# Kernel tuning notes

Hardware: AMD Instinct MI355X
Metric: run time of the kernel (lower is better)

Reference implementation:

```python
import jax, jax.numpy as jnp
import numpy as np

BS, T, HS, WS = 2, 4, 32, 32
HW = HS * WS
D, NH, NL, NP = 256, 8, 4, 4
HD = D // NH
DFFN = 1024


def layer_norm(x, g, b, eps=1e-5):
    mu = jnp.mean(x, axis=-1, keepdims=True)
    var = jnp.mean((x - mu) ** 2, axis=-1, keepdims=True)
    return (x - mu) * jax.lax.rsqrt(var + eps) * g + b


def bilinear_gather(val, loc, Hl, Wl):
    # val: (bs, nh, Hl*Wl, hd); loc: (bs, Lq, nh, P, 2) in [0,1], last dim (x, y)
    # matches F.grid_sample(align_corners=False, padding_mode='zeros') on grid=2*loc-1
    x = loc[..., 0] * Wl - 0.5
    y = loc[..., 1] * Hl - 0.5
    x0 = jnp.floor(x)
    y0 = jnp.floor(y)
    lx = x - x0
    ly = y - y0
    bs, Lq, nh, P = x.shape
    out = jnp.zeros((bs, nh, Lq * P, val.shape[-1]), val.dtype)
    for dy in (0, 1):
        for dx in (0, 1):
            xi = x0 + dx
            yi = y0 + dy
            w = (lx if dx else 1.0 - lx) * (ly if dy else 1.0 - ly)
            valid = (xi >= 0) & (xi < Wl) & (yi >= 0) & (yi < Hl)
            w = jnp.where(valid, w, 0.0)
            xi_c = jnp.clip(xi, 0, Wl - 1).astype(jnp.int32)
            yi_c = jnp.clip(yi, 0, Hl - 1).astype(jnp.int32)
            idx = (yi_c * Wl + xi_c).transpose(0, 2, 1, 3).reshape(bs, nh, Lq * P)
            g = jnp.take_along_axis(val, idx[..., None], axis=2)
            wt = w.transpose(0, 2, 1, 3).reshape(bs, nh, Lq * P)
            out = out + wt[..., None] * g
    return out.reshape(bs, nh, Lq, P, val.shape[-1])


def setup_inputs() -> dict:
    key = jax.random.key(0)
    ks = jax.random.split(key, 12)
    s = 0.02
    return {
        "src": jax.random.normal(ks[0], (BS, T, HW, D), jnp.float32),
        "pos": jax.random.normal(ks[1], (BS, T, HW, D), jnp.float32),
        "reference_points": jax.random.uniform(ks[2], (BS, T * HW, NL, 2), jnp.float32),
        "value_proj_w": jax.random.normal(ks[3], (D, D), jnp.float32) * s,
        "value_proj_b": jnp.zeros((D,), jnp.float32),
        "sampling_offsets_w": jax.random.normal(ks[4], (D, NH * NL * NP * 2), jnp.float32) * s,
        "sampling_offsets_b": jax.random.normal(ks[5], (NH * NL * NP * 2,), jnp.float32) * s,
        "attn_weights_w": jax.random.normal(ks[6], (D, NH * NL * NP), jnp.float32) * s,
        "attn_weights_b": jnp.zeros((NH * NL * NP,), jnp.float32),
        "output_proj_w": jax.random.normal(ks[7], (D, D), jnp.float32) * s,
        "output_proj_b": jnp.zeros((D,), jnp.float32),
        "norm1_g": jnp.ones((D,), jnp.float32),
        "norm1_b": jnp.zeros((D,), jnp.float32),
        "linear1_w": jax.random.normal(ks[8], (D, DFFN), jnp.float32) * s,
        "linear1_b": jnp.zeros((DFFN,), jnp.float32),
        "linear2_w": jax.random.normal(ks[9], (DFFN, D), jnp.float32) * s,
        "linear2_b": jnp.zeros((D,), jnp.float32),
        "norm2_g": jnp.ones((D,), jnp.float32),
        "norm2_b": jnp.zeros((D,), jnp.float32),
        "spatial_shapes": np.array([[HS, WS]] * NL, np.int32),
        "level_start_index": np.arange(NL, dtype=np.int32) * HW,
    }


def reference(src, pos, reference_points, value_proj_w, value_proj_b,
              sampling_offsets_w, sampling_offsets_b, attn_weights_w, attn_weights_b,
              output_proj_w, output_proj_b, norm1_g, norm1_b,
              linear1_w, linear1_b, linear2_w, linear2_b, norm2_g, norm2_b,
              spatial_shapes, level_start_index):
    bs, t, hw, d = src.shape
    Lq = t * hw
    x = src.reshape(bs, Lq, d)
    q = x  # module never adds pos in forward (with_pos_embed unused)
    value = (x @ value_proj_w + value_proj_b).reshape(bs, Lq, NH, HD)
    offsets = (q @ sampling_offsets_w + sampling_offsets_b).reshape(bs, Lq, NH, NL, NP, 2)
    aw = jax.nn.softmax((q @ attn_weights_w + attn_weights_b).reshape(bs, Lq, NH, NL * NP), axis=-1)
    aw = aw.reshape(bs, Lq, NH, NL, NP)
    ss = np.asarray(spatial_shapes)
    lsi = np.asarray(level_start_index)
    offset_normalizer = jnp.asarray(ss[:, ::-1].copy(), src.dtype)  # (L, 2) = (W, H)
    sampling_locations = reference_points[:, :, None, :, None, :] + offsets / offset_normalizer[None, None, None, :, None, :]
    attn_out = jnp.zeros((bs, NH, Lq, HD), src.dtype)
    for l in range(NL):
        Hl, Wl = int(ss[l, 0]), int(ss[l, 1])
        start = int(lsi[l])
        v_l = value[:, start:start + Hl * Wl].transpose(0, 2, 1, 3)  # (bs, nh, HlWl, hd)
        samp = bilinear_gather(v_l, sampling_locations[:, :, :, l], Hl, Wl)  # (bs, nh, Lq, P, hd)
        w_l = aw[:, :, :, l].transpose(0, 2, 1, 3)  # (bs, nh, Lq, P)
        attn_out = attn_out + jnp.sum(samp * w_l[..., None], axis=3)
    attn_out = attn_out.transpose(0, 2, 1, 3).reshape(bs, Lq, d) @ output_proj_w + output_proj_b
    x = layer_norm(x + attn_out, norm1_g, norm1_b)
    ffn = jax.nn.relu(x @ linear1_w + linear1_b) @ linear2_w + linear2_b
    x = layer_norm(x + ffn, norm2_g, norm2_b)
    return x.reshape(bs, t, hw, d), sampling_locations
```

## Files before the change

kernel.cpp:

```cpp
#include <hip/hip_runtime.h>
#include <math.h>

#define ROWS   8192
#define LQ     4096
#define NHEAD  8
#define NLVL   4
#define NPTS   4
#define HDIM   32

typedef __attribute__((ext_vector_type(8))) short v8s;
typedef __attribute__((ext_vector_type(4))) float v4f;
typedef __attribute__((ext_vector_type(8))) unsigned short v8u;

__device__ __forceinline__ unsigned short f2bf(float x) {
    unsigned int u = __float_as_uint(x);
    u += 0x7fffu + ((u >> 16) & 1u);
    return (unsigned short)(u >> 16);
}
__device__ __forceinline__ float bf2f(unsigned short x) {
    return __uint_as_float(((unsigned int)x) << 16);
}

__device__ __forceinline__ void glds16(const void* g, void* l) {
    __builtin_amdgcn_global_load_lds(
        (const __attribute__((address_space(1))) unsigned int*)g,
        (__attribute__((address_space(3))) unsigned int*)l, 16, 0, 0);
}

__device__ __forceinline__ void trans_tile(const float* __restrict__ in,
                                           unsigned short* __restrict__ out,
                                           int K, int N, int ldout, int n_off,
                                           int bx, int by, int tid)
{
    __shared__ float t[32][33];
    int tx = tid & 31, ty = tid >> 5;
    int k0 = by << 5, n0 = bx << 5;
    #pragma unroll
    for (int i = 0; i < 4; i++)
        t[ty + i * 8][tx] = in[(size_t)(k0 + ty + i * 8) * N + n0 + tx];
    __syncthreads();
    #pragma unroll
    for (int i = 0; i < 4; i++)
        out[(size_t)(n_off + n0 + ty + i * 8) * ldout + k0 + tx] = f2bf(t[tx][ty + i * 8]);
}

__global__ __launch_bounds__(256) void prep_k(
    const float* __restrict__ vw, const float* __restrict__ ofw,
    const float* __restrict__ aww, const float* __restrict__ pw,
    const float* __restrict__ w1, const float* __restrict__ w2,
    unsigned short* __restrict__ Btcat, unsigned short* __restrict__ pwT,
    unsigned short* __restrict__ w1T, unsigned short* __restrict__ w2T,
    const float* __restrict__ vb, const float* __restrict__ ofb,
    const float* __restrict__ awb, float* __restrict__ biascat)
{
    int bid = blockIdx.x, tid = threadIdx.x;
    if (bid < 64) {
        int t = bid; trans_tile(vw, Btcat, 256, 256, 256, 0, t & 7, t >> 3, tid);
    } else if (bid < 128) {
        int t = bid - 64; trans_tile(ofw, Btcat, 256, 256, 256, 256, t & 7, t >> 3, tid);
    } else if (bid < 160) {
        int t = bid - 128; trans_tile(aww, Btcat, 256, 128, 256, 512, t & 3, t >> 2, tid);
    } else if (bid < 224) {
        int t = bid - 160; trans_tile(pw, pwT, 256, 256, 256, 0, t & 7, t >> 3, tid);
    } else if (bid < 480) {
        int t = bid - 224; trans_tile(w1, w1T, 256, 1024, 256, 0, t & 31, t >> 5, tid);
    } else if (bid < 736) {
        int t = bid - 480; trans_tile(w2, w2T, 1024, 256, 1024, 0, t & 7, t >> 3, tid);
    } else {
        biascat[tid] = vb[tid];
        biascat[tid + 256] = ofb[tid];
        if (tid < 128) biascat[tid + 512] = awb[tid];
    }
}

template<bool PROJ, bool AF32, bool OUTBF, bool RELU, bool RES>
__global__ __launch_bounds__(256) void mfma_gemm128_k(
    const void* __restrict__ Araw,
    const unsigned short* __restrict__ Bt,
    const float* __restrict__ bias,
    const float* __restrict__ res,
    void* __restrict__ Cout,
    unsigned short* __restrict__ vbf,
    const float* __restrict__ refp,
    float* __restrict__ oloc,
    int M, int N, int K)
{
    __shared__ __align__(16) unsigned short As[2048];
    __shared__ __align__(16) unsigned short Bs[4096];
    const int tid = threadIdx.x;
    const int row0 = blockIdx.y << 6, col0 = blockIdx.x << 7;
    const int wid = tid >> 6, lane = tid & 63;
    const int wm = wid & 1, wn = wid >> 1;
    const int lr = lane & 15, kq = lane >> 4;

    v4f acc[2][4];
    #pragma unroll
    for (int i = 0; i < 2; i++)
        #pragma unroll
        for (int j = 0; j < 4; j++) acc[i][j] = (v4f){0.f, 0.f, 0.f, 0.f};

    for (int k0 = 0; k0 < K; k0 += 32) {
        float4 af0, af1;
        if constexpr (AF32) {
            const float* Af = (const float*)Araw;
            int r1 = tid >> 2, kk1 = ((tid & 3) + (r1 >> 2)) & 3;
            const float* p1 = Af + (size_t)(row0 + r1) * K + k0 + kk1 * 8;
            af0 = *(const float4*)p1; af1 = *(const float4*)(p1 + 4);
        }
        __syncthreads();
        if constexpr (AF32) {
            v8u u1;
            u1[0] = f2bf(af0.x); u1[1] = f2bf(af0.y); u1[2] = f2bf(af0.z); u1[3] = f2bf(af0.w);
            u1[4] = f2bf(af1.x); u1[5] = f2bf(af1.y); u1[6] = f2bf(af1.z); u1[7] = f2bf(af1.w);
            *(v8u*)(&As[tid * 8]) = u1;
        } else {
            const unsigned short* A = (const unsigned short*)Araw;
            int c = wid * 64 + lane;
            int row = c >> 2;
            int kk = ((c & 3) + (row >> 2)) & 3;
            glds16(A + (size_t)(row0 + row) * K + k0 + kk * 8,
                   &As[(wid * 64) * 8]);
        }
        #pragma unroll
        for (int i = 0; i < 2; i++) {
            int c = wid * 128 + i * 64 + lane;
            int row = c >> 2;
            int kk = ((c & 3) + (row >> 2)) & 3;
            glds16(Bt + (size_t)(col0 + row) * K + k0 + kk * 8,
                   &Bs[(wid * 128 + i * 64) * 8]);
        }
        __syncthreads();
        v8s bf[4];
        #pragma unroll
        for (int nt = 0; nt < 4; nt++) {
            int row = wn * 64 + nt * 16 + lr;
            int s = (kq - (row >> 2)) & 3;
            bf[nt] = *(const v8s*)(&Bs[(row * 4 + s) * 8]);
        }
        #pragma unroll
        for (int mt = 0; mt < 2; mt++) {
            int row = wm * 32 + mt * 16 + lr;
            int s = (kq - (row >> 2)) & 3;
            v8s af = *(const v8s*)(&As[(row * 4 + s) * 8]);
            #pragma unroll
            for (int nt = 0; nt < 4; nt++)
                acc[mt][nt] = __builtin_amdgcn_mfma_f32_16x16x32_bf16(af, bf[nt], acc[mt][nt], 0, 0, 0);
        }
    }

    const int rq = lane >> 4;
    #pragma unroll
    for (int mt = 0; mt < 2; mt++) {
        #pragma unroll
        for (int nt = 0; nt < 4; nt++) {
            int col = col0 + wn * 64 + nt * 16 + lr;
            float bv = bias[col];
            #pragma unroll
            for (int i = 0; i < 4; i++) {
                int row = row0 + wm * 32 + mt * 16 + rq * 4 + i;
                float v = acc[mt][nt][i] + bv;
                if (RELU) v = fmaxf(v, 0.f);
                if (RES)  v += res[(size_t)row * N + col];
                if (PROJ) {
                    if (col < 256) {
                        int b = row >> 12, rb = row & 4095;
                        int l = rb >> 10, pix = rb & 1023;
                        int h = col >> 5, d = col & 31;
                        size_t idx = ((size_t)(((b << 2) + l) * 8 + h) << 15) + (pix << 5) + d;
                        vbf[idx] = f2bf(v);
                    } else if (col < 512) {
                        int colm = col - 256;
                        int l = (colm >> 3) & 3, cc = colm & 1;
                        oloc[(size_t)row * 256 + colm] =
                            refp[(size_t)row * 8 + l * 2 + cc] + v * (1.f / 32.f);
                    } else {
                        ((float*)Cout)[(size_t)row * 128 + col - 512] = v;
                    }
                } else if (OUTBF) {
                    ((unsigned short*)Cout)[(size_t)row * N + col] = f2bf(v);
                } else {
                    ((float*)Cout)[(size_t)row * N + col] = v;
                }
            }
        }
    }
}

template<bool OUTBF, bool RELU, bool RES>
__global__ __launch_bounds__(256) void mfma_gemm64_k(
    const unsigned short* __restrict__ A,
    const unsigned short* __restrict__ Bt,
    const float* __restrict__ bias,
    const float* __restrict__ res,
    void* __restrict__ Cout,
    int M, int N, int K)
{
    __shared__ __align__(16) unsigned short As[2048];
    __shared__ __align__(16) unsigned short Bs[2048];
    const int tid = threadIdx.x;
    const int row0 = blockIdx.y << 6, col0 = blockIdx.x << 6;
    const int wid = tid >> 6, lane = tid & 63;
    const int lr = lane & 15, kq = lane >> 4;

    v4f acc[4];
    #pragma unroll
    for (int i = 0; i < 4; i++) acc[i] = (v4f){0.f, 0.f, 0.f, 0.f};

    for (int k0 = 0; k0 < K; k0 += 32) {
        __syncthreads();
        {
            int c = wid * 64 + lane;
            int row = c >> 2;
            int kk = ((c & 3) + (row >> 2)) & 3;
            glds16(A + (size_t)(row0 + row) * K + k0 + kk * 8, &As[wid * 512]);
            glds16(Bt + (size_t)(col0 + row) * K + k0 + kk * 8, &Bs[wid * 512]);
        }
        __syncthreads();
        int colr = wid * 16 + lr;
        int sb = (kq - (colr >> 2)) & 3;
        v8s bf = *(const v8s*)(&Bs[(colr * 4 + sb) * 8]);
        #pragma unroll
        for (int mt = 0; mt < 4; mt++) {
            int rowr = mt * 16 + lr;
            int sa = (kq - (rowr >> 2)) & 3;
            v8s af = *(const v8s*)(&As[(rowr * 4 + sa) * 8]);
            acc[mt] = __builtin_amdgcn_mfma_f32_16x16x32_bf16(af, bf, acc[mt], 0, 0, 0);
        }
    }

    const int rq = lane >> 4;
    const int col = col0 + wid * 16 + lr;
    float bv = bias[col];
    #pragma unroll
    for (int mt = 0; mt < 4; mt++) {
        #pragma unroll
        for (int i = 0; i < 4; i++) {
            int row = row0 + mt * 16 + rq * 4 + i;
            float v = acc[mt][i] + bv;
            if (RELU) v = fmaxf(v, 0.f);
            if (RES)  v += res[(size_t)row * N + col];
            if (OUTBF) ((unsigned short*)Cout)[(size_t)row * N + col] = f2bf(v);
            else       ((float*)Cout)[(size_t)row * N + col] = v;
        }
    }
}

template<bool WRITE_BF>
__global__ __launch_bounds__(256) void mfma_gemm_ln_k(
    const unsigned short* __restrict__ A,
    const unsigned short* __restrict__ Bt,
    const float* __restrict__ bias,
    const float* __restrict__ res,
    const float* __restrict__ g,
    const float* __restrict__ b,
    float* __restrict__ out,
    unsigned short* __restrict__ outbf,
    int M, int K)
{
    __shared__ __align__(16) unsigned short As[1024];
    __shared__ __align__(16) unsigned short Bs[8192];
    __shared__ float red[2][32][4];
    const int tid = threadIdx.x;
    const int row0 = blockIdx.x << 5;
    const int wid = tid >> 6, lane = tid & 63;
    const int lr = lane & 15, kq = lane >> 4;
    const int rq = kq;

    v4f acc[2][4];
    #pragma unroll
    for (int i = 0; i < 2; i++)
        #pragma unroll
        for (int j = 0; j < 4; j++) acc[i][j] = (v4f){0.f, 0.f, 0.f, 0.f};

    for (int k0 = 0; k0 < K; k0 += 32) {
        __syncthreads();
        if (wid < 2) {
            int c = wid * 64 + lane;
            int row = c >> 2;
            int kk = ((c & 3) + (row >> 2)) & 3;
            glds16(A + (size_t)(row0 + row) * K + k0 + kk * 8,
                   &As[(wid * 64) * 8]);
        }
        #pragma unroll
        for (int i = 0; i < 4; i++) {
            int c = (wid * 4 + i) * 64 + lane;
            int col = c >> 2;
            int kk = ((c & 3) + (col >> 2)) & 3;
            glds16(Bt + (size_t)col * K + k0 + kk * 8,
                   &Bs[((wid * 4 + i) * 64) * 8]);
        }
        __syncthreads();
        v8s bf[4];
        #pragma unroll
        for (int ct = 0; ct < 4; ct++) {
            int col = wid * 64 + ct * 16 + lr;
            int s = (kq - (col >> 2)) & 3;
            bf[ct] = *(const v8s*)(&Bs[(col * 4 + s) * 8]);
        }
        #pragma unroll
        for (int rt = 0; rt < 2; rt++) {
            int rowl = rt * 16 + lr;
            int s = (kq - (rowl >> 2)) & 3;
            v8s af = *(const v8s*)(&As[(rowl * 4 + s) * 8]);
            #pragma unroll
            for (int ct = 0; ct < 4; ct++)
                acc[rt][ct] = __builtin_amdgcn_mfma_f32_16x16x32_bf16(af, bf[ct], acc[rt][ct], 0, 0, 0);
        }
    }

    float t[2][4][4];
    float s1[2][4], s2[2][4];
    #pragma unroll
    for (int rt = 0; rt < 2; rt++)
        #pragma unroll
        for (int i = 0; i < 4; i++) { s1[rt][i] = 0.f; s2[rt][i] = 0.f; }
    #pragma unroll
    for (int rt = 0; rt < 2; rt++) {
        #pragma unroll
        for (int ct = 0; ct < 4; ct++) {
            int col = wid * 64 + ct * 16 + lr;
            float bv = bias[col];
            #pragma unroll
            for (int i = 0; i < 4; i++) {
                int row = row0 + rt * 16 + rq * 4 + i;
                float v = acc[rt][ct][i] + bv + res[(size_t)row * 256 + col];
                t[rt][ct][i] = v;
                s1[rt][i] += v;
                s2[rt][i] += v * v;
            }
        }
    }
    #pragma unroll
    for (int o = 1; o < 16; o <<= 1) {
        #pragma unroll
        for (int rt = 0; rt < 2; rt++)
            #pragma unroll
            for (int i = 0; i < 4; i++) {
                s1[rt][i] += __shfl_xor(s1[rt][i], o);
                s2[rt][i] += __shfl_xor(s2[rt][i], o);
            }
    }
    if (lr == 0) {
        #pragma unroll
        for (int rt = 0; rt < 2; rt++)
            #pragma unroll
            for (int i = 0; i < 4; i++) {
                int rl = rt * 16 + rq * 4 + i;
                red[0][rl][wid] = s1[rt][i];
                red[1][rl][wid] = s2[rt][i];
            }
    }
    __syncthreads();
    float mu[2][4], rstd[2][4];
    #pragma unroll
    for (int rt = 0; rt < 2; rt++) {
        #pragma unroll
        for (int i = 0; i < 4; i++) {
            int rl = rt * 16 + rq * 4 + i;
            float S1 = red[0][rl][0] + red[0][rl][1] + red[0][rl][2] + red[0][rl][3];
            float S2 = red[1][rl][0] + red[1][rl][1] + red[1][rl][2] + red[1][rl][3];
            float m = S1 * (1.f / 256.f);
            mu[rt][i] = m;
            rstd[rt][i] = rsqrtf(S2 * (1.f / 256.f) - m * m + 1e-5f);
        }
    }
    #pragma unroll
    for (int rt = 0; rt < 2; rt++) {
        #pragma unroll
        for (int ct = 0; ct < 4; ct++) {
            int col = wid * 64 + ct * 16 + lr;
            float gg = g[col], bb = b[col];
            #pragma unroll
            for (int i = 0; i < 4; i++) {
                int row = row0 + rt * 16 + rq * 4 + i;
                float o = (t[rt][ct][i] - mu[rt][i]) * rstd[rt][i] * gg + bb;
                out[(size_t)row * 256 + col] = o;
                if (WRITE_BF) outbf[(size_t)row * 256 + col] = f2bf(o);
            }
        }
    }
}

__global__ __launch_bounds__(256) void fused_gather_k(
    const float* __restrict__ po,
    const unsigned short* __restrict__ vbf,
    const float* __restrict__ loc,
    unsigned short* __restrict__ attn_bf)
{
    int tid = threadIdx.x;
    int g = tid >> 4, l = (tid >> 2) & 3, d8 = tid & 3;
    int h = blockIdx.x & 7;
    int r = (blockIdx.x >> 3) * 16 + g;
    int b = r >> 12;

    float locv[8];
    *(float4*)(locv)     = *(const float4*)(loc + (size_t)r * 256 + h * 32 + l * 8);
    *(float4*)(locv + 4) = *(const float4*)(loc + (size_t)r * 256 + h * 32 + l * 8 + 4);

    float w4[4];
    *(float4*)(w4) = *(const float4*)(po + (size_t)r * 128 + h * 16 + l * 4);
    float m = fmaxf(fmaxf(w4[0], w4[1]), fmaxf(w4[2], w4[3]));
    m = fmaxf(m, __shfl_xor(m, 4));
    m = fmaxf(m, __shfl_xor(m, 8));
    float s = 0.f;
    #pragma unroll
    for (int p = 0; p < 4; p++) { w4[p] = __expf(w4[p] - m); s += w4[p]; }
    s += __shfl_xor(s, 4);
    s += __shfl_xor(s, 8);
    float inv = 1.f / s;

    const unsigned short* vbase =
        vbf + (((size_t)(((b << 2) + l) * 8 + h)) << 15) + d8 * 8;

    float acc[8];
    #pragma unroll
    for (int k = 0; k < 8; k++) acc[k] = 0.f;

    #pragma unroll
    for (int pp = 0; pp < 2; pp++) {
        v8u uv[8];
        float cw[8];
        #pragma unroll
        for (int p2 = 0; p2 < 2; p2++) {
            int p = pp * 2 + p2;
            float xf = locv[p * 2] * 32.f - 0.5f, yf = locv[p * 2 + 1] * 32.f - 0.5f;
            float x0f = floorf(xf), y0f = floorf(yf);
            float fx = xf - x0f, fy = yf - y0f;
            int x0 = (int)x0f, y0 = (int)y0f;
            float wgt = w4[p] * inv;
            #pragma unroll
            for (int dy = 0; dy < 2; dy++) {
                #pragma unroll
                for (int dx = 0; dx < 2; dx++) {
                    int idx = p2 * 4 + dy * 2 + dx;
                    int xi = x0 + dx, yi = y0 + dy;
                    float wt = (dx ? fx : 1.f - fx) * (dy ? fy : 1.f - fy);
                    bool valid = (xi >= 0) & (xi < 32) & (yi >= 0) & (yi < 32);
                    int xc = min(max(xi, 0), 31), yc = min(max(yi, 0), 31);
                    cw[idx] = valid ? (wgt * wt) : 0.f;
                    uv[idx] = *(const v8u*)(vbase + (size_t)((yc << 5) + xc) * 32);
                }
            }
        }
        #pragma unroll
        for (int idx = 0; idx < 8; idx++) {
            float c = cw[idx];
            #pragma unroll
            for (int k = 0; k < 8; k++)
                acc[k] += c * bf2f(uv[idx][k]);
        }
    }
    #pragma unroll
    for (int k = 0; k < 8; k++) {
        acc[k] += __shfl_xor(acc[k], 4);
        acc[k] += __shfl_xor(acc[k], 8);
    }
    if (l == 0) {
        v8u o;
        #pragma unroll
        for (int k = 0; k < 8; k++) o[k] = f2bf(acc[k]);
        *(v8u*)(attn_bf + (size_t)r * 256 + h * 32 + d8 * 8) = o;
    }
}

template<bool WRITE_BF>
__global__ __launch_bounds__(256) void layernorm_k(
    float* __restrict__ x, const float* __restrict__ g, const float* __restrict__ b,
    unsigned short* __restrict__ xbf)
{
    int lane = threadIdx.x & 63;
    int wv = threadIdx.x >> 6;
    int row = blockIdx.x * 4 + wv;
    int c = lane << 2;
    float4 v = *(const float4*)(x + (size_t)row * 256 + c);
    float s = v.x + v.y + v.z + v.w;
    #pragma unroll
    for (int o = 1; o < 64; o <<= 1) s += __shfl_xor(s, o);
    float mu = s * (1.f / 256.f);
    float d0 = v.x - mu, d1 = v.y - mu, d2 = v.z - mu, d3 = v.w - mu;
    float vs = d0 * d0 + d1 * d1 + d2 * d2 + d3 * d3;
    #pragma unroll
    for (int o = 1; o < 64; o <<= 1) vs += __shfl_xor(vs, o);
    float rstd = rsqrtf(vs * (1.f / 256.f) + 1e-5f);
    float4 gg = *(const float4*)(g + c);
    float4 bb = *(const float4*)(b + c);
    float4 o4;
    o4.x = d0 * rstd * gg.x + bb.x;
    o4.y = d1 * rstd * gg.y + bb.y;
    o4.z = d2 * rstd * gg.z + bb.z;
    o4.w = d3 * rstd * gg.w + bb.w;
    *(float4*)(x + (size_t)row * 256 + c) = o4;
    if (WRITE_BF) {
        ushort4 ob;
        ob.x = f2bf(o4.x); ob.y = f2bf(o4.y); ob.z = f2bf(o4.z); ob.w = f2bf(o4.w);
        *(ushort4*)(xbf + (size_t)row * 256 + c) = ob;
    }
}

extern "C" void kernel_launch(void* const* d_in, const int* in_sizes, int n_in,
                              void* d_out, int out_size, void* d_ws, size_t ws_size,
                              hipStream_t stream)
{
    const float* src   = (const float*)d_in[0];
    const float* refp  = (const float*)d_in[2];
    const float* vw    = (const float*)d_in[3];
    const float* vb    = (const float*)d_in[4];
    const float* ofw   = (const float*)d_in[5];
    const float* ofb   = (const float*)d_in[6];
    const float* aww   = (const float*)d_in[7];
    const float* awb   = (const float*)d_in[8];
    const float* pw    = (const float*)d_in[9];
    const float* pb    = (const float*)d_in[10];
    const float* g1    = (const float*)d_in[11];
    const float* b1    = (const float*)d_in[12];
    const float* w1    = (const float*)d_in[13];
    const float* bi1   = (const float*)d_in[14];
    const float* w2    = (const float*)d_in[15];
    const float* bi2   = (const float*)d_in[16];
    const float* g2    = (const float*)d_in[17];
    const float* b2    = (const float*)d_in[18];

    float* ws = (float*)d_ws;
    float*          po        = ws;
    float*          x1        = ws + 1048576;
    unsigned short* value_bf  = (unsigned short*)(ws + 3145728);
    unsigned short* x1_bf     = (unsigned short*)(ws + 5242880);
    unsigned short* attn_bf   = (unsigned short*)(ws + 6291456);
    unsigned short* hidden_bf = (unsigned short*)(ws + 7340032);
    unsigned short* Btcat     = (unsigned short*)(ws + 11534336);
    unsigned short* pwT       = (unsigned short*)(ws + 11616256);
    unsigned short* w1T       = (unsigned short*)(ws + 11649024);
    unsigned short* w2T       = (unsigned short*)(ws + 11780096);
    float*          biascat   = ws + 11911168;

    float* out_x   = (float*)d_out;
    float* out_loc = out_x + 2097152;

    dim3 blk(256);

    prep_k<<<737, blk, 0, stream>>>(vw, ofw, aww, pw, w1, w2,
                                    Btcat, pwT, w1T, w2T, vb, ofb, awb, biascat);

    mfma_gemm128_k<true, true, false, false, false><<<dim3(5, 128), blk, 0, stream>>>(
        src, Btcat, biascat, nullptr, po, value_bf, refp, out_loc, ROWS, 640, 256);

    fused_gather_k<<<4096, blk, 0, stream>>>(po, value_bf, out_loc, attn_bf);

    mfma_gemm_ln_k<true><<<256, blk, 0, stream>>>(
        attn_bf, pwT, pb, src, g1, b1, x1, x1_bf, ROWS, 256);

    mfma_gemm128_k<false, false, true, true, false><<<dim3(8, 128), blk, 0, stream>>>(
        x1_bf, w1T, bi1, nullptr, hidden_bf, nullptr, nullptr, nullptr, ROWS, 1024, 256);

    mfma_gemm64_k<false, false, true><<<dim3(4, 128), blk, 0, stream>>>(
        hidden_bf, w2T, bi2, x1, out_x, ROWS, 256, 1024);
    layernorm_k<false><<<2048, blk, 0, stream>>>(out_x, g2, b2, nullptr);
}
```

Measured before the change: 182.0 us.

## Merge kernel chain into two cooperative persistent kernels with grid syncs

Replaces six of the seven separate launches with two cooperative kernels of 512 blocks. The first does the weight transposes and the fused input projection, separated by a grid barrier. The second runs out-proj+LN1, FFN1, FFN2 and LN2 with grid barriers between stages. The aim is to remove launch gaps and tail effects between small kernels. In exchange, the fixed 512-block grid limits parallelism for stages that previously used more blocks. The kernels also carry the combined shared memory of all their phases, which may cut occupancy and co-residency.

New measurement: 681.5 us. 275% more time.

```diff
diff --git a/kernel.cpp b/kernel.cpp
--- a/kernel.cpp
+++ b/kernel.cpp
@@ -1,12 +1,10 @@
 #include <hip/hip_runtime.h>
+#include <hip/hip_cooperative_groups.h>
 #include <math.h>
 
+namespace cg = cooperative_groups;
+
 #define ROWS   8192
-#define LQ     4096
-#define NHEAD  8
-#define NLVL   4
-#define NPTS   4
-#define HDIM   32
 
 typedef __attribute__((ext_vector_type(8))) short v8s;
 typedef __attribute__((ext_vector_type(4))) float v4f;
@@ -44,51 +42,16 @@
         out[(size_t)(n_off + n0 + ty + i * 8) * ldout + k0 + tx] = f2bf(t[tx][ty + i * 8]);
 }
 
-__global__ __launch_bounds__(256) void prep_k(
-    const float* __restrict__ vw, const float* __restrict__ ofw,
-    const float* __restrict__ aww, const float* __restrict__ pw,
-    const float* __restrict__ w1, const float* __restrict__ w2,
-    unsigned short* __restrict__ Btcat, unsigned short* __restrict__ pwT,
-    unsigned short* __restrict__ w1T, unsigned short* __restrict__ w2T,
-    const float* __restrict__ vb, const float* __restrict__ ofb,
-    const float* __restrict__ awb, float* __restrict__ biascat)
-{
-    int bid = blockIdx.x, tid = threadIdx.x;
-    if (bid < 64) {
-        int t = bid; trans_tile(vw, Btcat, 256, 256, 256, 0, t & 7, t >> 3, tid);
-    } else if (bid < 128) {
-        int t = bid - 64; trans_tile(ofw, Btcat, 256, 256, 256, 256, t & 7, t >> 3, tid);
-    } else if (bid < 160) {
-        int t = bid - 128; trans_tile(aww, Btcat, 256, 128, 256, 512, t & 3, t >> 2, tid);
-    } else if (bid < 224) {
-        int t = bid - 160; trans_tile(pw, pwT, 256, 256, 256, 0, t & 7, t >> 3, tid);
-    } else if (bid < 480) {
-        int t = bid - 224; trans_tile(w1, w1T, 256, 1024, 256, 0, t & 31, t >> 5, tid);
-    } else if (bid < 736) {
-        int t = bid - 480; trans_tile(w2, w2T, 1024, 256, 1024, 0, t & 7, t >> 3, tid);
-    } else {
-        biascat[tid] = vb[tid];
-        biascat[tid + 256] = ofb[tid];
-        if (tid < 128) biascat[tid + 512] = awb[tid];
-    }
-}
-
-template<bool PROJ, bool AF32, bool OUTBF, bool RELU, bool RES>
-__global__ __launch_bounds__(256) void mfma_gemm128_k(
-    const void* __restrict__ Araw,
-    const unsigned short* __restrict__ Bt,
-    const float* __restrict__ bias,
-    const float* __restrict__ res,
-    void* __restrict__ Cout,
-    unsigned short* __restrict__ vbf,
-    const float* __restrict__ refp,
-    float* __restrict__ oloc,
-    int M, int N, int K)
+__device__ __forceinline__ void proj_tile(
+    const float* __restrict__ Af, const unsigned short* __restrict__ Bt,
+    const float* __restrict__ bias, float* __restrict__ po,
+    unsigned short* __restrict__ vbf, const float* __restrict__ refp,
+    float* __restrict__ oloc, int bx, int by, int tid)
 {
     __shared__ __align__(16) unsigned short As[2048];
     __shared__ __align__(16) unsigned short Bs[4096];
-    const int tid = threadIdx.x;
-    const int row0 = blockIdx.y << 6, col0 = blockIdx.x << 7;
+    const int K = 256;
+    const int row0 = by << 6, col0 = bx << 7;
     const int wid = tid >> 6, lane = tid & 63;
     const int wm = wid & 1, wn = wid >> 1;
     const int lr = lane & 15, kq = lane >> 4;
@@ -100,27 +63,15 @@
         for (int j = 0; j < 4; j++) acc[i][j] = (v4f){0.f, 0.f, 0.f, 0.f};
 
     for (int k0 = 0; k0 < K; k0 += 32) {
-        float4 af0, af1;
-        if constexpr (AF32) {
-            const float* Af = (const float*)Araw;
-            int r1 = tid >> 2, kk1 = ((tid & 3) + (r1 >> 2)) & 3;
-            const float* p1 = Af + (size_t)(row0 + r1) * K + k0 + kk1 * 8;
-            af0 = *(const float4*)p1; af1 = *(const float4*)(p1 + 4);
-        }
-        __syncthreads();
-        if constexpr (AF32) {
-            v8u u1;
-            u1[0] = f2bf(af0.x); u1[1] = f2bf(af0.y); u1[2] = f2bf(af0.z); u1[3] = f2bf(af0.w);
-            u1[4] = f2bf(af1.x); u1[5] = f2bf(af1.y); u1[6] = f2bf(af1.z); u1[7] = f2bf(af1.w);
-            *(v8u*)(&As[tid * 8]) = u1;
-        } else {
-            const unsigned short* A = (const unsigned short*)Araw;
-            int c = wid * 64 + lane;
-            int row = c >> 2;
-            int kk = ((c & 3) + (row >> 2)) & 3;
-            glds16(A + (size_t)(row0 + row) * K + k0 + kk * 8,
-                   &As[(wid * 64) * 8]);
-        }
+        int r1 = tid >> 2, kk1 = ((tid & 3) + (r1 >> 2)) & 3;
+        const float* p1 = Af + (size_t)(row0 + r1) * K + k0 + kk1 * 8;
+        float4 af0 = *(const float4*)p1;
+        float4 af1 = *(const float4*)(p1 + 4);
+        __syncthreads();
+        v8u u1;
+        u1[0] = f2bf(af0.x); u1[1] = f2bf(af0.y); u1[2] = f2bf(af0.z); u1[3] = f2bf(af0.w);
+        u1[4] = f2bf(af1.x); u1[5] = f2bf(af1.y); u1[6] = f2bf(af1.z); u1[7] = f2bf(af1.w);
+        *(v8u*)(&As[tid * 8]) = u1;
         #pragma unroll
         for (int i = 0; i < 2; i++) {
             int c = wid * 128 + i * 64 + lane;
@@ -159,52 +110,43 @@
             for (int i = 0; i < 4; i++) {
                 int row = row0 + wm * 32 + mt * 16 + rq * 4 + i;
                 float v = acc[mt][nt][i] + bv;
-                if (RELU) v = fmaxf(v, 0.f);
-                if (RES)  v += res[(size_t)row * N + col];
-                if (PROJ) {
-                    if (col < 256) {
-                        int b = row >> 12, rb = row & 4095;
-                        int l = rb >> 10, pix = rb & 1023;
-                        int h = col >> 5, d = col & 31;
-                        size_t idx = ((size_t)(((b << 2) + l) * 8 + h) << 15) + (pix << 5) + d;
-                        vbf[idx] = f2bf(v);
-                    } else if (col < 512) {
-                        int colm = col - 256;
-                        int l = (colm >> 3) & 3, cc = colm & 1;
-                        oloc[(size_t)row * 256 + colm] =
-                            refp[(size_t)row * 8 + l * 2 + cc] + v * (1.f / 32.f);
-                    } else {
-                        ((float*)Cout)[(size_t)row * 128 + col - 512] = v;
-                    }
-                } else if (OUTBF) {
-                    ((unsigned short*)Cout)[(size_t)row * N + col] = f2bf(v);
+                if (col < 256) {
+                    int b = row >> 12, rb = row & 4095;
+                    int l = rb >> 10, pix = rb & 1023;
+                    int h = col >> 5, d = col & 31;
+                    size_t idx = ((size_t)(((b << 2) + l) * 8 + h) << 15) + (pix << 5) + d;
+                    vbf[idx] = f2bf(v);
+                } else if (col < 512) {
+                    int colm = col - 256;
+                    int l = (colm >> 3) & 3, cc = colm & 1;
+                    oloc[(size_t)row * 256 + colm] =
+                        refp[(size_t)row * 8 + l * 2 + cc] + v * (1.f / 32.f);
                 } else {
-                    ((float*)Cout)[(size_t)row * N + col] = v;
+                    po[(size_t)row * 128 + col - 512] = v;
                 }
             }
         }
     }
 }
 
-template<bool OUTBF, bool RELU, bool RES>
-__global__ __launch_bounds__(256) void mfma_gemm64_k(
-    const unsigned short* __restrict__ A,
-    const unsigned short* __restrict__ Bt,
-    const float* __restrict__ bias,
-    const float* __restrict__ res,
-    void* __restrict__ Cout,
-    int M, int N, int K)
-{
-    __shared__ __align__(16) unsigned short As[2048];
-    __shared__ __align__(16) unsigned short Bs[2048];
-    const int tid = threadIdx.x;
-    const int row0 = blockIdx.y << 6, col0 = blockIdx.x << 6;
+__device__ __forceinline__ void ffn1_tile(
+    const unsigned short* __restrict__ A, const unsigned short* __restrict__ Bt,
+    const float* __restrict__ bias, unsigned short* __restrict__ Cout,
+    int bx, int by, int tid)
+{
+    __shared__ __align__(16) unsigned short As1[2048];
+    __shared__ __align__(16) unsigned short Bs1[4096];
+    const int K = 256, N = 1024;
+    const int row0 = by << 6, col0 = bx << 7;
     const int wid = tid >> 6, lane = tid & 63;
+    const int wm = wid & 1, wn = wid >> 1;
     const int lr = lane & 15, kq = lane >> 4;
 
-    v4f acc[4];
-    #pragma unroll
-    for (int i = 0; i < 4; i++) acc[i] = (v4f){0.f, 0.f, 0.f, 0.f};
+    v4f acc[2][4];
+    #pragma unroll
+    for (int i = 0; i < 2; i++)
+        #pragma unroll
+        for (int j = 0; j < 4; j++) acc[i][j] = (v4f){0.f, 0.f, 0.f, 0.f};
 
     for (int k0 = 0; k0 < K; k0 += 32) {
         __syncthreads();
@@ -212,18 +154,86 @@
             int c = wid * 64 + lane;
             int row = c >> 2;
             int kk = ((c & 3) + (row >> 2)) & 3;
-            glds16(A + (size_t)(row0 + row) * K + k0 + kk * 8, &As[wid * 512]);
-            glds16(Bt + (size_t)(col0 + row) * K + k0 + kk * 8, &Bs[wid * 512]);
+            glds16(A + (size_t)(row0 + row) * K + k0 + kk * 8, &As1[(wid * 64) * 8]);
+        }
+        #pragma unroll
+        for (int i = 0; i < 2; i++) {
+            int c = wid * 128 + i * 64 + lane;
+            int row = c >> 2;
+            int kk = ((c & 3) + (row >> 2)) & 3;
+            glds16(Bt + (size_t)(col0 + row) * K + k0 + kk * 8,
+                   &Bs1[(wid * 128 + i * 64) * 8]);
+        }
+        __syncthreads();
+        v8s bf[4];
+        #pragma unroll
+        for (int nt = 0; nt < 4; nt++) {
+            int row = wn * 64 + nt * 16 + lr;
+            int s = (kq - (row >> 2)) & 3;
+            bf[nt] = *(const v8s*)(&Bs1[(row * 4 + s) * 8]);
+        }
+        #pragma unroll
+        for (int mt = 0; mt < 2; mt++) {
+            int row = wm * 32 + mt * 16 + lr;
+            int s = (kq - (row >> 2)) & 3;
+            v8s af = *(const v8s*)(&As1[(row * 4 + s) * 8]);
+            #pragma unroll
+            for (int nt = 0; nt < 4; nt++)
+                acc[mt][nt] = __builtin_amdgcn_mfma_f32_16x16x32_bf16(af, bf[nt], acc[mt][nt], 0, 0, 0);
+        }
+    }
+
+    const int rq = lane >> 4;
+    #pragma unroll
+    for (int mt = 0; mt < 2; mt++) {
+        #pragma unroll
+        for (int nt = 0; nt < 4; nt++) {
+            int col = col0 + wn * 64 + nt * 16 + lr;
+            float bv = bias[col];
+            #pragma unroll
+            for (int i = 0; i < 4; i++) {
+                int row = row0 + wm * 32 + mt * 16 + rq * 4 + i;
+                float v = fmaxf(acc[mt][nt][i] + bv, 0.f);
+                Cout[(size_t)row * N + col] = f2bf(v);
+            }
+        }
+    }
+}
+
+__device__ __forceinline__ void ffn2_tile(
+    const unsigned short* __restrict__ A, const unsigned short* __restrict__ Bt,
+    const float* __restrict__ bias, const float* __restrict__ res,
+    float* __restrict__ Cout, int bx, int by, int tid)
+{
+    __shared__ __align__(16) unsigned short As2[2048];
+    __shared__ __align__(16) unsigned short Bs2[2048];
+    const int K = 1024, N = 256;
+    const int row0 = by << 6, col0 = bx << 6;
+    const int wid = tid >> 6, lane = tid & 63;
+    const int lr = lane & 15, kq = lane >> 4;
+
+    v4f acc[4];
+    #pragma unroll
+    for (int i = 0; i < 4; i++) acc[i] = (v4f){0.f, 0.f, 0.f, 0.f};
+
+    for (int k0 = 0; k0 < K; k0 += 32) {
+        __syncthreads();
+        {
+            int c = wid * 64 + lane;
+            int row = c >> 2;
+            int kk = ((c & 3) + (row >> 2)) & 3;
+            glds16(A + (size_t)(row0 + row) * K + k0 + kk * 8, &As2[wid * 512]);
+            glds16(Bt + (size_t)(col0 + row) * K + k0 + kk * 8, &Bs2[wid * 512]);
         }
         __syncthreads();
         int colr = wid * 16 + lr;
         int sb = (kq - (colr >> 2)) & 3;
-        v8s bf = *(const v8s*)(&Bs[(colr * 4 + sb) * 8]);
+        v8s bf = *(const v8s*)(&Bs2[(colr * 4 + sb) * 8]);
         #pragma unroll
         for (int mt = 0; mt < 4; mt++) {
             int rowr = mt * 16 + lr;
             int sa = (kq - (rowr >> 2)) & 3;
-            v8s af = *(const v8s*)(&As[(rowr * 4 + sa) * 8]);
+            v8s af = *(const v8s*)(&As2[(rowr * 4 + sa) * 8]);
             acc[mt] = __builtin_amdgcn_mfma_f32_16x16x32_bf16(af, bf, acc[mt], 0, 0, 0);
         }
     }
@@ -236,32 +246,24 @@
         #pragma unroll
         for (int i = 0; i < 4; i++) {
             int row = row0 + mt * 16 + rq * 4 + i;
-            float v = acc[mt][i] + bv;
-            if (RELU) v = fmaxf(v, 0.f);
-            if (RES)  v += res[(size_t)row * N + col];
-            if (OUTBF) ((unsigned short*)Cout)[(size_t)row * N + col] = f2bf(v);
-            else       ((float*)Cout)[(size_t)row * N + col] = v;
-        }
-    }
-}
-
-template<bool WRITE_BF>
-__global__ __launch_bounds__(256) void mfma_gemm_ln_k(
-    const unsigned short* __restrict__ A,
-    const unsigned short* __restrict__ Bt,
-    const float* __restrict__ bias,
-    const float* __restrict__ res,
-    const float* __restrict__ g,
-    const float* __restrict__ b,
-    float* __restrict__ out,
-    unsigned short* __restrict__ outbf,
-    int M, int K)
-{
-    __shared__ __align__(16) unsigned short As[1024];
-    __shared__ __align__(16) unsigned short Bs[8192];
+            float v = acc[mt][i] + bv + res[(size_t)row * N + col];
+            Cout[(size_t)row * N + col] = v;
+        }
+    }
+}
+
+__device__ __forceinline__ void outproj_ln_tile(
+    const unsigned short* __restrict__ A, const unsigned short* __restrict__ Bt,
+    const float* __restrict__ bias, const float* __restrict__ res,
+    const float* __restrict__ g, const float* __restrict__ b,
+    float* __restrict__ out, unsigned short* __restrict__ outbf,
+    int bxy, int tid)
+{
+    __shared__ __align__(16) unsigned short As3[1024];
+    __shared__ __align__(16) unsigned short Bs3[8192];
     __shared__ float red[2][32][4];
-    const int tid = threadIdx.x;
-    const int row0 = blockIdx.x << 5;
+    const int K = 256;
+    const int row0 = bxy << 5;
     const int wid = tid >> 6, lane = tid & 63;
     const int lr = lane & 15, kq = lane >> 4;
     const int rq = kq;
@@ -278,16 +280,14 @@
             int c = wid * 64 + lane;
             int row = c >> 2;
             int kk = ((c & 3) + (row >> 2)) & 3;
-            glds16(A + (size_t)(row0 + row) * K + k0 + kk * 8,
-                   &As[(wid * 64) * 8]);
+            glds16(A + (size_t)(row0 + row) * K + k0 + kk * 8, &As3[(wid * 64) * 8]);
         }
         #pragma unroll
         for (int i = 0; i < 4; i++) {
             int c = (wid * 4 + i) * 64 + lane;
             int col = c >> 2;
             int kk = ((c & 3) + (col >> 2)) & 3;
-            glds16(Bt + (size_t)col * K + k0 + kk * 8,
-                   &Bs[((wid * 4 + i) * 64) * 8]);
+            glds16(Bt + (size_t)col * K + k0 + kk * 8, &Bs3[((wid * 4 + i) * 64) * 8]);
         }
         __syncthreads();
         v8s bf[4];
@@ -295,13 +295,13 @@
         for (int ct = 0; ct < 4; ct++) {
             int col = wid * 64 + ct * 16 + lr;
             int s = (kq - (col >> 2)) & 3;
-            bf[ct] = *(const v8s*)(&Bs[(col * 4 + s) * 8]);
+            bf[ct] = *(const v8s*)(&Bs3[(col * 4 + s) * 8]);
         }
         #pragma unroll
         for (int rt = 0; rt < 2; rt++) {
             int rowl = rt * 16 + lr;
             int s = (kq - (rowl >> 2)) & 3;
-            v8s af = *(const v8s*)(&As[(rowl * 4 + s) * 8]);
+            v8s af = *(const v8s*)(&As3[(rowl * 4 + s) * 8]);
             #pragma unroll
             for (int ct = 0; ct < 4; ct++)
                 acc[rt][ct] = __builtin_amdgcn_mfma_f32_16x16x32_bf16(af, bf[ct], acc[rt][ct], 0, 0, 0);
@@ -375,10 +375,93 @@
                 int row = row0 + rt * 16 + rq * 4 + i;
                 float o = (t[rt][ct][i] - mu[rt][i]) * rstd[rt][i] * gg + bb;
                 out[(size_t)row * 256 + col] = o;
-                if (WRITE_BF) outbf[(size_t)row * 256 + col] = f2bf(o);
+                outbf[(size_t)row * 256 + col] = f2bf(o);
             }
         }
     }
+}
+
+__device__ __forceinline__ void ln_rows(float* __restrict__ x,
+                                        const float* __restrict__ g,
+                                        const float* __restrict__ b,
+                                        int t, int tid)
+{
+    int lane = tid & 63;
+    int wv = tid >> 6;
+    int row = t * 4 + wv;
+    int c = lane << 2;
+    float4 v = *(const float4*)(x + (size_t)row * 256 + c);
+    float s = v.x + v.y + v.z + v.w;
+    #pragma unroll
+    for (int o = 1; o < 64; o <<= 1) s += __shfl_xor(s, o);
+    float mu = s * (1.f / 256.f);
+    float d0 = v.x - mu, d1 = v.y - mu, d2 = v.z - mu, d3 = v.w - mu;
+    float vs = d0 * d0 + d1 * d1 + d2 * d2 + d3 * d3;
+    #pragma unroll
+    for (int o = 1; o < 64; o <<= 1) vs += __shfl_xor(vs, o);
+    float rstd = rsqrtf(vs * (1.f / 256.f) + 1e-5f);
+    float4 gg = *(const float4*)(g + c);
+    float4 bb = *(const float4*)(b + c);
+    float4 o4;
+    o4.x = d0 * rstd * gg.x + bb.x;
+    o4.y = d1 * rstd * gg.y + bb.y;
+    o4.z = d2 * rstd * gg.z + bb.z;
+    o4.w = d3 * rstd * gg.w + bb.w;
+    *(float4*)(x + (size_t)row * 256 + c) = o4;
+}
+
+__global__ __launch_bounds__(256, 2) void coopA_k(
+    const float* src,
+    const float* vw, const float* ofw, const float* aww, const float* pw,
+    const float* w1, const float* w2,
+    unsigned short* Btcat, unsigned short* pwT,
+    unsigned short* w1T, unsigned short* w2T,
+    const float* vb, const float* ofb, const float* awb, float* biascat,
+    float* po, unsigned short* vbf, const float* refp, float* oloc)
+{
+    int bid = blockIdx.x, tid = threadIdx.x;
+    for (int t = bid; t < 737; t += 512) {
+        if (t < 64) { trans_tile(vw, Btcat, 256, 256, 256, 0, t & 7, t >> 3, tid); }
+        else if (t < 128) { int u = t - 64;  trans_tile(ofw, Btcat, 256, 256, 256, 256, u & 7, u >> 3, tid); }
+        else if (t < 160) { int u = t - 128; trans_tile(aww, Btcat, 256, 128, 256, 512, u & 3, u >> 2, tid); }
+        else if (t < 224) { int u = t - 160; trans_tile(pw, pwT, 256, 256, 256, 0, u & 7, u >> 3, tid); }
+        else if (t < 480) { int u = t - 224; trans_tile(w1, w1T, 256, 1024, 256, 0, u & 31, u >> 5, tid); }
+        else if (t < 736) { int u = t - 480; trans_tile(w2, w2T, 1024, 256, 1024, 0, u & 7, u >> 3, tid); }
+        else {
+            biascat[tid] = vb[tid];
+            biascat[tid + 256] = ofb[tid];
+            if (tid < 128) biascat[tid + 512] = awb[tid];
+        }
+        __syncthreads();
+    }
+    __threadfence();
+    cg::this_grid().sync();
+    for (int t = bid; t < 640; t += 512)
+        proj_tile(src, Btcat, biascat, po, vbf, refp, oloc, t % 5, t / 5, tid);
+}
+
+__global__ __launch_bounds__(256, 2) void coopC_k(
+    const unsigned short* attn_bf, const unsigned short* pwT, const float* pb,
+    const float* src, const float* g1, const float* b1,
+    float* x1, unsigned short* x1_bf,
+    const unsigned short* w1T, const float* bi1, unsigned short* hidden_bf,
+    const unsigned short* w2T, const float* bi2, float* out_x,
+    const float* g2, const float* b2)
+{
+    int bid = blockIdx.x, tid = threadIdx.x;
+    if (bid < 256)
+        outproj_ln_tile(attn_bf, pwT, pb, src, g1, b1, x1, x1_bf, bid, tid);
+    __threadfence();
+    cg::this_grid().sync();
+    for (int t = bid; t < 1024; t += 512)
+        ffn1_tile(x1_bf, w1T, bi1, hidden_bf, t % 8, t / 8, tid);
+    __threadfence();
+    cg::this_grid().sync();
+    ffn2_tile(hidden_bf, w2T, bi2, x1, out_x, bid % 4, bid / 4, tid);
+    __threadfence();
+    cg::this_grid().sync();
+    for (int t = bid; t < 2048; t += 512)
+        ln_rows(out_x, g2, b2, t, tid);
 }
 
 __global__ __launch_bounds__(256) void fused_gather_k(
@@ -460,40 +543,6 @@
         #pragma unroll
         for (int k = 0; k < 8; k++) o[k] = f2bf(acc[k]);
         *(v8u*)(attn_bf + (size_t)r * 256 + h * 32 + d8 * 8) = o;
-    }
-}
-
-template<bool WRITE_BF>
-__global__ __launch_bounds__(256) void layernorm_k(
-    float* __restrict__ x, const float* __restrict__ g, const float* __restrict__ b,
-    unsigned short* __restrict__ xbf)
-{
-    int lane = threadIdx.x & 63;
-    int wv = threadIdx.x >> 6;
-    int row = blockIdx.x * 4 + wv;
-    int c = lane << 2;
-    float4 v = *(const float4*)(x + (size_t)row * 256 + c);
-    float s = v.x + v.y + v.z + v.w;
-    #pragma unroll
-    for (int o = 1; o < 64; o <<= 1) s += __shfl_xor(s, o);
-    float mu = s * (1.f / 256.f);
-    float d0 = v.x - mu, d1 = v.y - mu, d2 = v.z - mu, d3 = v.w - mu;
-    float vs = d0 * d0 + d1 * d1 + d2 * d2 + d3 * d3;
-    #pragma unroll
-    for (int o = 1; o < 64; o <<= 1) vs += __shfl_xor(vs, o);
-    float rstd = rsqrtf(vs * (1.f / 256.f) + 1e-5f);
-    float4 gg = *(const float4*)(g + c);
-    float4 bb = *(const float4*)(b + c);
-    float4 o4;
-    o4.x = d0 * rstd * gg.x + bb.x;
-    o4.y = d1 * rstd * gg.y + bb.y;
-    o4.z = d2 * rstd * gg.z + bb.z;
-    o4.w = d3 * rstd * gg.w + bb.w;
-    *(float4*)(x + (size_t)row * 256 + c) = o4;
-    if (WRITE_BF) {
-        ushort4 ob;
-        ob.x = f2bf(o4.x); ob.y = f2bf(o4.y); ob.z = f2bf(o4.z); ob.w = f2bf(o4.w);
-        *(ushort4*)(xbf + (size_t)row * 256 + c) = ob;
     }
 }
 
@@ -536,23 +585,23 @@
     float* out_x   = (float*)d_out;
     float* out_loc = out_x + 2097152;
 
-    dim3 blk(256);
-
-    prep_k<<<737, blk, 0, stream>>>(vw, ofw, aww, pw, w1, w2,
-                                    Btcat, pwT, w1T, w2T, vb, ofb, awb, biascat);
-
-    mfma_gemm128_k<true, true, false, false, false><<<dim3(5, 128), blk, 0, stream>>>(
-        src, Btcat, biascat, nullptr, po, value_bf, refp, out_loc, ROWS, 640, 256);
-
-    fused_gather_k<<<4096, blk, 0, stream>>>(po, value_bf, out_loc, attn_bf);
-
-    mfma_gemm_ln_k<true><<<256, blk, 0, stream>>>(
-        attn_bf, pwT, pb, src, g1, b1, x1, x1_bf, ROWS, 256);
-
-    mfma_gemm128_k<false, false, true, true, false><<<dim3(8, 128), blk, 0, stream>>>(
-        x1_bf, w1T, bi1, nullptr, hidden_bf, nullptr, nullptr, nullptr, ROWS, 1024, 256);
-
-    mfma_gemm64_k<false, false, true><<<dim3(4, 128), blk, 0, stream>>>(
-        hidden_bf, w2T, bi2, x1, out_x, ROWS, 256, 1024);
-    layernorm_k<false><<<2048, blk, 0, stream>>>(out_x, g2, b2, nullptr);
-}
+    void* argsA[] = {
+        (void*)&src, (void*)&vw, (void*)&ofw, (void*)&aww, (void*)&pw,
+        (void*)&w1, (void*)&w2, (void*)&Btcat, (void*)&pwT, (void*)&w1T,
+        (void*)&w2T, (void*)&vb, (void*)&ofb, (void*)&awb, (void*)&biascat,
+        (void*)&po, (void*)&value_bf, (void*)&refp, (void*)&out_loc
+    };
+    hipLaunchCooperativeKernel((const void*)coopA_k, dim3(512), dim3(256),
+                               argsA, 0, stream);
+
+    fused_gather_k<<<4096, dim3(256), 0, stream>>>(po, value_bf, out_loc, attn_bf);
+
+    void* argsC[] = {
+        (void*)&attn_bf, (void*)&pwT, (void*)&pb, (void*)&src, (void*)&g1,
+        (void*)&b1, (void*)&x1, (void*)&x1_bf, (void*)&w1T, (void*)&bi1,
+        (void*)&hidden_bf, (void*)&w2T, (void*)&bi2, (void*)&out_x,
+        (void*)&g2, (void*)&b2
+    };
+    hipLaunchCooperativeKernel((const void*)coopC_k, dim3(512), dim3(256),
+                               argsC, 0, stream);
+}
```
